# Optimization experiments

Hardware: AMD Instinct MI355X
Metric: run time of the kernel (lower is better)

The kernel has to match this reference:

```python
import jax, jax.numpy as jnp
import numpy as np

B = 2          # point clouds per batch
N_PER = 80000  # occupied voxels per cloud
D = 64         # voxel grid resolution
K = 27         # 3x3x3 kernel volume
EPS = 1e-5


def _build_maps():
    rng = np.random.RandomState(0)
    coords = []
    for b in range(B):
        flat = rng.choice(D ** 3, N_PER, replace=False)
        x = flat // (D * D); y = (flat // D) % D; z = flat % D
        coords.append(np.stack([np.full(N_PER, b, np.int64), x, y, z], 1))
    coords = np.concatenate(coords, 0)  # [N,4] (batch, x, y, z)

    def make_grid(c, Dd):
        g = np.full(B * Dd ** 3, -1, np.int64)
        key = ((c[:, 0] * Dd + c[:, 1]) * Dd + c[:, 2]) * Dd + c[:, 3]
        g[key] = np.arange(len(c))
        return g

    offsets = np.array([[dx, dy, dz] for dx in (-1, 0, 1) for dy in (-1, 0, 1) for dz in (-1, 0, 1)], np.int64)

    def kernel_map(c, g, Dd):
        # per kernel offset: (input_row, output_row) pairs, padded to M with sentinel n
        n = len(c)
        ins, outs = [], []
        for off in offsets:
            sc = c[:, 1:] + off
            valid = np.all((sc >= 0) & (sc < Dd), 1)
            key = ((c[:, 0] * Dd + sc[:, 0]) * Dd + sc[:, 1]) * Dd + sc[:, 2]
            row = np.where(valid, g[np.clip(key, 0, len(g) - 1)], -1)
            m = row >= 0
            ins.append(row[m]); outs.append(np.nonzero(m)[0])
        M = max(len(a) for a in ins)
        ki = np.full((K, M), n, np.int32); ko = np.full((K, M), n, np.int32)
        for k in range(K):
            ki[k, :len(ins[k])] = ins[k]; ko[k, :len(outs[k])] = outs[k]
        return ki, ko

    km_in, km_out = kernel_map(coords, make_grid(coords, D), D)

    # maxpool k2/s2: each voxel maps to exactly one pooled coordinate floor(c/2)
    Dp = D // 2
    pc = coords.copy(); pc[:, 1:] //= 2
    pkey = ((pc[:, 0] * Dp + pc[:, 1]) * Dp + pc[:, 2]) * Dp + pc[:, 3]
    ukey, pool_seg = np.unique(pkey, return_inverse=True)
    pz = ukey % Dp; py = (ukey // Dp) % Dp; px = (ukey // (Dp * Dp)) % Dp; pb = ukey // (Dp ** 3)
    pcoords = np.stack([pb, px, py, pz], 1)
    km2_in, km2_out = kernel_map(pcoords, make_grid(pcoords, Dp), Dp)
    return len(coords), len(pcoords), km_in, km_out, pool_seg.astype(np.int32), km2_in, km2_out


N, N_POOL, _KM_IN, _KM_OUT, _POOL_SEG, _KM2_IN, _KM2_OUT = _build_maps()


def setup_inputs() -> dict:
    key = jax.random.key(0)
    ks = jax.random.split(key, 4)
    f32 = jnp.float32
    return {
        "feats": jax.random.normal(ks[0], (N, 1), f32),
        "W1": jax.random.normal(ks[1], (K, 1, 64), f32) * 0.2,
        "b1": jnp.zeros((64,), f32),
        "g1": jnp.ones((64,), f32), "be1": jnp.zeros((64,), f32),
        "W2": jax.random.normal(ks[2], (K, 64, 64), f32) * 0.05,
        "b2": jnp.zeros((64,), f32),
        "g2": jnp.ones((64,), f32), "be2": jnp.zeros((64,), f32),
        "W3": jax.random.normal(ks[3], (K, 64, 128), f32) * 0.05,
        "b3": jnp.zeros((128,), f32),
        "g3": jnp.ones((128,), f32), "be3": jnp.zeros((128,), f32),
        "km_in": jnp.asarray(_KM_IN), "km_out": jnp.asarray(_KM_OUT),
        "pool_seg": jnp.asarray(_POOL_SEG),
        "km2_in": jnp.asarray(_KM2_IN), "km2_out": jnp.asarray(_KM2_OUT),
    }


def _sparse_conv(x, ki, ko, W, b):
    # gather-GEMM-scatter per kernel offset; sentinel index n hits padded zero row / dummy out row
    n = x.shape[0]
    xp = jnp.concatenate([x, jnp.zeros((1, x.shape[1]), x.dtype)], 0)
    out = jnp.zeros((n + 1, W.shape[2]), x.dtype)
    for k in range(K):
        out = out.at[ko[k]].add(xp[ki[k]] @ W[k])
    return out[:n] + b


def _bn_relu(x, g, b):
    # training-mode BatchNorm over all active voxels (biased variance), then ReLU
    mu = jnp.mean(x, 0)
    var = jnp.mean((x - mu) ** 2, 0)
    return jax.nn.relu(g * (x - mu) * jax.lax.rsqrt(var + EPS) + b)


def reference(feats, W1, b1, g1, be1, W2, b2, g2, be2, W3, b3, g3, be3,
              km_in, km_out, pool_seg, km2_in, km2_out):
    x = _bn_relu(_sparse_conv(feats, km_in, km_out, W1, b1), g1, be1)
    x = _bn_relu(_sparse_conv(x, km_in, km_out, W2, b2), g2, be2)
    # maxpool k2/s2: segment-max onto pooled coordinates
    x = jnp.full((N_POOL, x.shape[1]), -jnp.inf, x.dtype).at[pool_seg].max(x)
    x = _bn_relu(_sparse_conv(x, km2_in, km2_out, W3, b3), g3, be3)
    return x  # [N_POOL, 128]
```

## Files before the change

### kernel.cpp

```cpp
#include <hip/hip_runtime.h>

#define EPS 1e-5f
#define KK 27

typedef __bf16 bf16x8 __attribute__((ext_vector_type(8)));
typedef float f32x4 __attribute__((ext_vector_type(4)));

__device__ __forceinline__ unsigned short f2bf(float f) {
    union { float f; unsigned u; } v; v.f = f;
    unsigned r = v.u + 0x7fffu + ((v.u >> 16) & 1u);
    return (unsigned short)(r >> 16);
}
__device__ __forceinline__ float bf2f(unsigned short h) {
    union { unsigned u; float f; } v; v.u = ((unsigned)h) << 16; return v.f;
}

__device__ __forceinline__ f32x4 mfma16(bf16x8 a, bf16x8 b, f32x4 c) {
    return __builtin_amdgcn_mfma_f32_16x16x32_bf16(a, b, c, 0, 0, 0);
}

__global__ void fill_i32(int* __restrict__ p, long tot, int val) {
    long i = (long)blockIdx.x * blockDim.x + threadIdx.x;
    if (i < tot) p[i] = val;
}

__global__ void invert_map_g(const int* __restrict__ km_in, const int* __restrict__ km_out,
                             int* __restrict__ idxG, int M, int nrows) {
    long i = (long)blockIdx.x * blockDim.x + threadIdx.x;
    if (i >= (long)KK * M) return;
    int k = (int)(i / M);
    int ki = km_in[i];
    if (ki < nrows) {
        int ko = km_out[i];
        idxG[(long)(ko >> 5) * 1024 + k * 32 + (ko & 31)] = ki;
    }
}

__global__ void wt_frag(const float* __restrict__ W, unsigned short* __restrict__ Wt,
                        int Cin, int Cout) {
    long i = (long)blockIdx.x * blockDim.x + threadIdx.x;
    long tot = (long)KK * Cin * Cout;
    if (i >= tot) return;
    int k  = (int)(i / (Cin * Cout));
    int r  = (int)(i % (Cin * Cout));
    int ci = r / Cout, co = r % Cout;
    int t = co >> 4, m16 = co & 15;
    int s = ci >> 5, quad = (ci >> 3) & 3, j = ci & 7;
    int lane = quad * 16 + m16;
    long off = ((((long)k * (Cout >> 4) + t) * 2 + s) * 64 + lane) * 8 + j;
    Wt[off] = f2bf(W[i]);
}

__global__ void w1t_bf16(const float* __restrict__ W1, unsigned short* __restrict__ W1t) {
    int i = blockIdx.x * blockDim.x + threadIdx.x;
    if (i >= 64 * 32) return;
    int c = i / 32, kk = i % 32;
    W1t[i] = (kk < KK) ? f2bf(W1[kk * 64 + c]) : (unsigned short)0;
}

__global__ void stats_part(const float* __restrict__ p, int nblk, int width,
                           float* __restrict__ out) {
    int c = threadIdx.x;
    int b0 = blockIdx.x * 64;
    int b1 = b0 + 64 < nblk ? b0 + 64 : nblk;
    float acc = 0.f;
    for (int b = b0; b < b1; ++b) acc += p[(long)b * width + c];
    atomicAdd(&out[c], acc);
}

__global__ __launch_bounds__(256, 2) void conv1_mfma(const float* __restrict__ feats,
                                                     const unsigned short* __restrict__ W1t,
                                                     const int* __restrict__ idxG, int n,
                                                     unsigned short* __restrict__ out,
                                                     float* __restrict__ partial) {
    __shared__ __align__(16) int lidx[4][1024];
    __shared__ float sstat[4][128];
    int tid = threadIdx.x;
    int wave = tid >> 6, lane = tid & 63;
    int m16 = lane & 15, quad = lane >> 4;
    long tile = (long)blockIdx.x * 4 + wave;
    long j0 = tile * 32;
    bool valid = (j0 < n);
    long jb = valid ? (j0 >> 5) : 0;

    {
        float* z = (float*)sstat;
        #pragma unroll
        for (int i = 0; i < 2; ++i) z[tid + i * 256] = 0.f;
    }
    __syncthreads();

    {
        const int* src = idxG + jb * 1024;
        #pragma unroll
        for (int i = 0; i < 4; ++i)
            __builtin_amdgcn_global_load_lds(
                (const __attribute__((address_space(1))) unsigned*)(src + i * 256 + lane * 4),
                (__attribute__((address_space(3))) unsigned*)(&lidx[wave][i * 256]),
                16, 0, 0);
    }
    asm volatile("s_waitcnt vmcnt(0)" ::: "memory");
    const int* lip = &lidx[wave][0];

    int idx[2][8];
    #pragma unroll
    for (int i = 0; i < 8; ++i) {
        int kk = quad * 8 + i;
        bool kv = (kk < KK);
        idx[0][i] = (valid && kv) ? lip[kk * 32 + m16] : n;
        idx[1][i] = (valid && kv) ? lip[kk * 32 + 16 + m16] : n;
    }
    float f[2][8];
    #pragma unroll
    for (int i = 0; i < 8; ++i)
        #pragma unroll
        for (int t2 = 0; t2 < 2; ++t2) {
            int r = idx[t2][i];
            f[t2][i] = (r < n) ? feats[r] : 0.f;
        }

    union { bf16x8 v; unsigned short s[8]; } a[2];
    #pragma unroll
    for (int t2 = 0; t2 < 2; ++t2)
        #pragma unroll
        for (int i = 0; i < 8; ++i) a[t2].s[i] = f2bf(f[t2][i]);

    f32x4 acc[2][4];
    #pragma unroll
    for (int t2 = 0; t2 < 2; ++t2)
        #pragma unroll
        for (int t = 0; t < 4; ++t) acc[t2][t] = (f32x4){0.f, 0.f, 0.f, 0.f};

    const unsigned short* wb = W1t + quad * 8;
    #pragma unroll
    for (int t = 0; t < 4; ++t) {
        bf16x8 b = *(const bf16x8*)(wb + (t * 16 + m16) * 32);
        acc[0][t] = mfma16(a[0].v, b, acc[0][t]);
        acc[1][t] = mfma16(a[1].v, b, acc[1][t]);
    }

    asm volatile("" ::: "memory");
    unsigned short* sb = (unsigned short*)&lidx[wave][0];
    #pragma unroll
    for (int t2 = 0; t2 < 2; ++t2)
        #pragma unroll
        for (int t = 0; t < 4; ++t)
            #pragma unroll
            for (int r2 = 0; r2 < 4; ++r2)
                sb[(t2 * 16 + quad * 4 + r2) * 64 + t * 16 + m16] = f2bf(acc[t2][t][r2]);
    asm volatile("s_waitcnt lgkmcnt(0)" ::: "memory");
    #pragma unroll
    for (int i = 0; i < 4; ++i) {
        int row = i * 8 + (lane >> 3);
        long rr = j0 + row;
        if (rr < n)
            *(bf16x8*)(out + rr * 64 + (lane & 7) * 8) =
                *(const bf16x8*)(sb + row * 64 + (lane & 7) * 8);
    }

    #pragma unroll
    for (int t = 0; t < 4; ++t) {
        float s = 0.f, q = 0.f;
        #pragma unroll
        for (int t2 = 0; t2 < 2; ++t2)
            #pragma unroll
            for (int r2 = 0; r2 < 4; ++r2) { float v = acc[t2][t][r2]; s += v; q += v * v; }
        s += __shfl_xor(s, 16); q += __shfl_xor(q, 16);
        s += __shfl_xor(s, 32); q += __shfl_xor(q, 32);
        if (quad == 0) {
            sstat[wave][t * 16 + m16] = s;
            sstat[wave][64 + t * 16 + m16] = q;
        }
    }
    __syncthreads();
    if (tid < 128) {
        float p = sstat[0][tid] + sstat[1][tid] + sstat[2][tid] + sstat[3][tid];
        partial[(long)blockIdx.x * 128 + tid] = p;
    }
}

__global__ void bnrelu1_vec(unsigned short* __restrict__ x, const float* __restrict__ stats,
                            const float* __restrict__ g, const float* __restrict__ be, long n) {
    __shared__ float sc[64], sh[64];
    int tid = threadIdx.x;
    if (tid < 64) {
        float mu  = stats[tid] / (float)n;
        float var = stats[64 + tid] / (float)n - mu * mu;
        float s   = g[tid] * rsqrtf(var + EPS);
        sc[tid] = s; sh[tid] = be[tid] - mu * s;
    }
    __syncthreads();
    long i = (long)blockIdx.x * 256 + tid;
    long tot = (n + 1) * 8;
    if (i >= tot) return;
    long j = i >> 3; int c0 = (int)(i & 7) * 8;
    union { bf16x8 v; unsigned short s[8]; } u, o;
    if (j < n) {
        u.v = *(const bf16x8*)(x + j * 64 + c0);
        #pragma unroll
        for (int t = 0; t < 8; ++t) {
            float f = bf2f(u.s[t]) * sc[c0 + t] + sh[c0 + t];
            o.s[t] = f2bf(f > 0.f ? f : 0.f);
        }
    } else {
        #pragma unroll
        for (int t = 0; t < 8; ++t) o.s[t] = 0;
    }
    *(bf16x8*)(x + j * 64 + c0) = o.v;
}

template <int NCG, bool BF16OUT>
__global__ __launch_bounds__(256, 2) void conv64(const unsigned short* __restrict__ xin,
                                                 const unsigned short* __restrict__ Wt,
                                                 const int* __restrict__ idxG,
                                                 void* __restrict__ outv, int n,
                                                 float* __restrict__ partial) {
    constexpr int NT = 4;
    constexpr int COUTF = 64 * NCG;
    constexpr int SW = 2 * COUTF;
    constexpr long KSLICE = (long)COUTF * 128;
    __shared__ __align__(16) int lidx[4][2][1024];
    __shared__ float sstat[4][SW];

    int tid = threadIdx.x;
    int wave = tid >> 6, lane = tid & 63;
    int m16 = lane & 15, quad = lane >> 4;
    long gw = (long)blockIdx.x * 4 + wave;
    long tile = (NCG == 2) ? (gw >> 1) : gw;
    int cg = (NCG == 2) ? (int)(gw & 1) : 0;
    long j0 = tile * 64;
    bool v0 = (j0 < n), v1 = (j0 + 32 < n);
    long jb0 = v0 ? (j0 >> 5) : 0;
    long jb1 = v1 ? ((j0 >> 5) + 1) : 0;

    {
        float* z = (float*)sstat;
        #pragma unroll
        for (int i = 0; i < (4 * SW + 255) / 256; ++i) {
            int o = tid + i * 256;
            if (o < 4 * SW) z[o] = 0.f;
        }
    }
    __syncthreads();

    {
        const int* s0 = idxG + jb0 * 1024;
        const int* s1 = idxG + jb1 * 1024;
        #pragma unroll
        for (int i = 0; i < 4; ++i) {
            __builtin_amdgcn_global_load_lds(
                (const __attribute__((address_space(1))) unsigned*)(s0 + i * 256 + lane * 4),
                (__attribute__((address_space(3))) unsigned*)(&lidx[wave][0][i * 256]),
                16, 0, 0);
            __builtin_amdgcn_global_load_lds(
                (const __attribute__((address_space(1))) unsigned*)(s1 + i * 256 + lane * 4),
                (__attribute__((address_space(3))) unsigned*)(&lidx[wave][1][i * 256]),
                16, 0, 0);
        }
    }
    asm volatile("s_waitcnt vmcnt(0)" ::: "memory");
    const int* lip0 = &lidx[wave][0][m16];
    const int* lip1 = &lidx[wave][1][m16];

    const char* wlane = (const char*)Wt + (long)cg * (NT * 2048) + (long)lane * 16;
    const unsigned short* xq = xin + quad * 8;

    bf16x8 bB[2][8];
    bf16x8 aA[2][8];

    auto issueB = [&](int k, int ph) {
        const char* wk = wlane + (long)k * KSLICE;
        #pragma unroll
        for (int f = 0; f < 8; ++f)
            bB[ph][f] = *(const bf16x8*)(wk + f * 1024);
    };
    auto issueA = [&](int r00, int r01, int r10, int r11, int ph) {
        const unsigned short* a;
        a = xq + (long)r00 * 64; aA[ph][0] = *(const bf16x8*)a; aA[ph][1] = *(const bf16x8*)(a + 32);
        a = xq + (long)r01 * 64; aA[ph][2] = *(const bf16x8*)a; aA[ph][3] = *(const bf16x8*)(a + 32);
        a = xq + (long)r10 * 64; aA[ph][4] = *(const bf16x8*)a; aA[ph][5] = *(const bf16x8*)(a + 32);
        a = xq + (long)r11 * 64; aA[ph][6] = *(const bf16x8*)a; aA[ph][7] = *(const bf16x8*)(a + 32);
    };

    {
        int r00 = v0 ? lip0[0] : n, r01 = v0 ? lip0[16] : n;
        int r10 = v1 ? lip1[0] : n, r11 = v1 ? lip1[16] : n;
        issueB(0, 0); issueA(r00, r01, r10, r11, 0);
        r00 = v0 ? lip0[32] : n; r01 = v0 ? lip0[48] : n;
        r10 = v1 ? lip1[32] : n; r11 = v1 ? lip1[48] : n;
        issueB(1, 1); issueA(r00, r01, r10, r11, 1);
    }

    f32x4 acc[2][2][NT];
    #pragma unroll
    for (int u = 0; u < 2; ++u)
        #pragma unroll
        for (int h = 0; h < 2; ++h)
            #pragma unroll
            for (int t = 0; t < NT; ++t) acc[u][h][t] = (f32x4){0.f, 0.f, 0.f, 0.f};

    #pragma unroll
    for (int k = 0; k < KK; ++k) {
        int r00 = n, r01 = n, r10 = n, r11 = n;
        if (k + 2 < KK) {
            r00 = v0 ? lip0[(k + 2) * 32] : n;
            r01 = v0 ? lip0[(k + 2) * 32 + 16] : n;
            r10 = v1 ? lip1[(k + 2) * 32] : n;
            r11 = v1 ? lip1[(k + 2) * 32 + 16] : n;
        }
        if (k < KK - 1) asm volatile("s_waitcnt vmcnt(16)" ::: "memory");
        else            asm volatile("s_waitcnt vmcnt(0)" ::: "memory");
        __builtin_amdgcn_s_setprio(1);
        #pragma unroll
        for (int s = 0; s < 2; ++s)
            #pragma unroll
            for (int t = 0; t < NT; ++t) {
                bf16x8 b = bB[k & 1][t * 2 + s];
                acc[0][0][t] = mfma16(aA[k & 1][0 + s], b, acc[0][0][t]);
                acc[0][1][t] = mfma16(aA[k & 1][2 + s], b, acc[0][1][t]);
                acc[1][0][t] = mfma16(aA[k & 1][4 + s], b, acc[1][0][t]);
                acc[1][1][t] = mfma16(aA[k & 1][6 + s], b, acc[1][1][t]);
            }
        __builtin_amdgcn_s_setprio(0);
        if (k + 2 < KK) {
            issueB(k + 2, k & 1);
            issueA(r00, r01, r10, r11, k & 1);
        }
    }

    asm volatile("" ::: "memory");
    #pragma unroll
    for (int u = 0; u < 2; ++u) {
        if (BF16OUT) {
            unsigned short* sb = (unsigned short*)&lidx[wave][0][0];
            #pragma unroll
            for (int h = 0; h < 2; ++h)
                #pragma unroll
                for (int t = 0; t < NT; ++t)
                    #pragma unroll
                    for (int r2 = 0; r2 < 4; ++r2)
                        sb[(h * 16 + quad * 4 + r2) * 64 + t * 16 + m16] = f2bf(acc[u][h][t][r2]);
            asm volatile("s_waitcnt lgkmcnt(0)" ::: "memory");
            #pragma unroll
            for (int i = 0; i < 4; ++i) {
                int row = i * 8 + (lane >> 3);
                long rr = j0 + u * 32 + row;
                if (rr < n)
                    *(bf16x8*)((unsigned short*)outv + rr * 64 + (lane & 7) * 8) =
                        *(const bf16x8*)(sb + row * 64 + (lane & 7) * 8);
            }
            asm volatile("" ::: "memory");
        } else {
            float* sb = (float*)&lidx[wave][0][0];
            #pragma unroll
            for (int h = 0; h < 2; ++h)
                #pragma unroll
                for (int t = 0; t < NT; ++t)
                    #pragma unroll
                    for (int r2 = 0; r2 < 4; ++r2)
                        sb[(h * 16 + quad * 4 + r2) * 64 + t * 16 + m16] = acc[u][h][t][r2];
            asm volatile("s_waitcnt lgkmcnt(0)" ::: "memory");
            #pragma unroll
            for (int i = 0; i < 8; ++i) {
                int row = i * 4 + (lane >> 4);
                long rr = j0 + u * 32 + row;
                if (rr < n)
                    *(float4*)((float*)outv + rr * COUTF + cg * 64 + (lane & 15) * 4) =
                        *(const float4*)(sb + row * 64 + (lane & 15) * 4);
            }
            asm volatile("" ::: "memory");
        }
    }

    #pragma unroll
    for (int t = 0; t < NT; ++t) {
        float s = 0.f, q = 0.f;
        #pragma unroll
        for (int u = 0; u < 2; ++u)
            #pragma unroll
            for (int h = 0; h < 2; ++h)
                #pragma unroll
                for (int r2 = 0; r2 < 4; ++r2) { float v = acc[u][h][t][r2]; s += v; q += v * v; }
        s += __shfl_xor(s, 16); q += __shfl_xor(q, 16);
        s += __shfl_xor(s, 32); q += __shfl_xor(q, 32);
        if (quad == 0) {
            sstat[wave][cg * 64 + t * 16 + m16] = s;
            sstat[wave][COUTF + cg * 64 + t * 16 + m16] = q;
        }
    }
    __syncthreads();
    if (tid < SW) {
        float p = sstat[0][tid] + sstat[1][tid] + sstat[2][tid] + sstat[3][tid];
        partial[(long)blockIdx.x * SW + tid] = p;
    }
}

__global__ void pool_kernel(const unsigned short* __restrict__ x, const float* __restrict__ stats,
                            const float* __restrict__ g, const float* __restrict__ be,
                            const int* __restrict__ seg, long n, unsigned* __restrict__ pooled) {
    long j = (long)blockIdx.x * 4 + threadIdx.y;
    if (j >= n) return;
    int c = threadIdx.x;
    float mu  = stats[c] / (float)n;
    float var = stats[64 + c] / (float)n - mu * mu;
    float rs  = rsqrtf(var + EPS);
    float v   = g[c] * (bf2f(x[j * 64 + c]) - mu) * rs + be[c];
    if (v < 0.f) v = 0.f;
    atomicMax(&pooled[(long)seg[j] * 64 + c], __float_as_uint(v));
}

__global__ void pooled_bf16_vec(const unsigned* __restrict__ pooled, long np,
                                unsigned short* __restrict__ out) {
    long i = (long)blockIdx.x * 256 + threadIdx.x;
    long tot = (np + 1) * 8;
    if (i >= tot) return;
    long j = i >> 3; int c0 = (int)(i & 7) * 8;
    union { bf16x8 v; unsigned short s[8]; } o;
    if (j < np) {
        #pragma unroll
        for (int t = 0; t < 8; ++t)
            o.s[t] = f2bf(__uint_as_float(pooled[j * 64 + c0 + t]));
    } else {
        #pragma unroll
        for (int t = 0; t < 8; ++t) o.s[t] = 0;
    }
    *(bf16x8*)(out + j * 64 + c0) = o.v;
}

__global__ void bnrelu_out_vec(float* __restrict__ x, const float* __restrict__ stats,
                               const float* __restrict__ g, const float* __restrict__ be,
                               long n) {
    __shared__ float sc[128], sh[128];
    int tid = threadIdx.x;
    if (tid < 128) {
        float mu  = stats[tid] / (float)n;
        float var = stats[128 + tid] / (float)n - mu * mu;
        float s   = g[tid] * rsqrtf(var + EPS);
        sc[tid] = s; sh[tid] = be[tid] - mu * s;
    }
    __syncthreads();
    long i = (long)blockIdx.x * 256 + tid;
    long tot = n * 32;
    if (i >= tot) return;
    int c0 = (int)(i & 31) * 4;
    float4 v = ((float4*)x)[i];
    v.x = v.x * sc[c0]     + sh[c0];     v.x = v.x > 0.f ? v.x : 0.f;
    v.y = v.y * sc[c0 + 1] + sh[c0 + 1]; v.y = v.y > 0.f ? v.y : 0.f;
    v.z = v.z * sc[c0 + 2] + sh[c0 + 2]; v.z = v.z > 0.f ? v.z : 0.f;
    v.w = v.w * sc[c0 + 3] + sh[c0 + 3]; v.w = v.w > 0.f ? v.w : 0.f;
    ((float4*)x)[i] = v;
}

extern "C" void kernel_launch(void* const* d_in, const int* in_sizes, int n_in,
                              void* d_out, int out_size, void* d_ws, size_t ws_size,
                              hipStream_t stream) {
    const float* feats = (const float*)d_in[0];
    const float* W1  = (const float*)d_in[1];
    const float* g1  = (const float*)d_in[3];
    const float* be1 = (const float*)d_in[4];
    const float* W2  = (const float*)d_in[5];
    const float* g2  = (const float*)d_in[7];
    const float* be2 = (const float*)d_in[8];
    const float* W3  = (const float*)d_in[9];
    const float* g3  = (const float*)d_in[11];
    const float* be3 = (const float*)d_in[12];
    const int* km_in   = (const int*)d_in[13];
    const int* km_out  = (const int*)d_in[14];
    const int* pool_seg = (const int*)d_in[15];
    const int* km2_in  = (const int*)d_in[16];
    const int* km2_out = (const int*)d_in[17];

    const int n  = in_sizes[0];
    const int M  = in_sizes[13] / KK;
    const int np = out_size / 128;
    const int M2 = in_sizes[16] / KK;
    const long nb1 = n / 32 + 2;
    const long nb2 = np / 32 + 2;

    const int waves1 = (n + 31) / 32;
    const int nblk1  = (waves1 + 3) / 4;
    const int waves2 = (n + 63) / 64;
    const int nblk2  = (waves2 + 3) / 4;
    const int waves3 = ((np + 63) / 64) * 2;
    const int nblk3  = (waves3 + 3) / 4;


    char* ws = (char*)d_ws;
    size_t off = 0;
    auto alloc = [&](size_t bytes) -> char* {
        char* p = ws + off;
        off += (bytes + 255) & ~(size_t)255;
        return p;
    };
    int* idxG1 = (int*)alloc(nb1 * 4096);
    int* idxG2 = (int*)alloc(nb2 * 4096);
    unsigned short* W1t = (unsigned short*)alloc(64 * 32 * 2);
    unsigned short* W2t = (unsigned short*)alloc((size_t)KK * 64 * 64 * 2);
    unsigned short* W3t = (unsigned short*)alloc((size_t)KK * 128 * 64 * 2);
    float* stats = (float*)alloc(4096);
    unsigned short* x1n = (unsigned short*)alloc((size_t)(n + 1) * 64 * 2);
    unsigned short* x2r = (unsigned short*)alloc((size_t)n * 64 * 2);
    unsigned* pooled = (unsigned*)alloc((size_t)np * 64 * 4);
    unsigned short* xpn = (unsigned short*)alloc((size_t)(np + 1) * 64 * 2);
    float* part1 = (float*)alloc((size_t)nblk1 * 128 * 4);
    float* part2 = (float*)alloc((size_t)nblk2 * 128 * 4);
    float* part3 = (float*)alloc((size_t)nblk3 * 256 * 4);
    float* x3 = (float*)d_out;
    if (off > ws_size) return;

    float* stats1 = stats;
    float* stats2 = stats + 128;
    float* stats3 = stats + 256;

    hipMemsetAsync(stats, 0, 4096, stream);
    hipMemsetAsync(pooled, 0, (size_t)np * 64 * 4, stream);

    {
        long t1 = nb1 * 1024;
        fill_i32<<<(int)((t1 + 255) / 256), 256, 0, stream>>>(idxG1, t1, n);
        long t2 = nb2 * 1024;
        fill_i32<<<(int)((t2 + 255) / 256), 256, 0, stream>>>(idxG2, t2, np);
        long e1 = (long)KK * M;
        invert_map_g<<<(int)((e1 + 255) / 256), 256, 0, stream>>>(km_in, km_out, idxG1, M, n);
        long e2 = (long)KK * M2;
        invert_map_g<<<(int)((e2 + 255) / 256), 256, 0, stream>>>(km2_in, km2_out, idxG2, M2, np);
    }
    {
        w1t_bf16<<<8, 256, 0, stream>>>(W1, W1t);
        long t2 = (long)KK * 64 * 64;
        wt_frag<<<(int)((t2 + 255) / 256), 256, 0, stream>>>(W2, W2t, 64, 64);
        long t3 = (long)KK * 64 * 128;
        wt_frag<<<(int)((t3 + 255) / 256), 256, 0, stream>>>(W3, W3t, 64, 128);
    }

    conv1_mfma<<<nblk1, 256, 0, stream>>>(feats, W1t, idxG1, n, x1n, part1);
    stats_part<<<(nblk1 + 63) / 64, 128, 0, stream>>>(part1, nblk1, 128, stats1);
    {
        long tot = ((long)(n + 1) * 8 + 255) / 256;
        bnrelu1_vec<<<(int)tot, 256, 0, stream>>>(x1n, stats1, g1, be1, n);
    }
    conv64<1, true><<<nblk2, 256, 0, stream>>>(x1n, W2t, idxG1, x2r, n, part2);
    stats_part<<<(nblk2 + 63) / 64, 128, 0, stream>>>(part2, nblk2, 128, stats2);
    pool_kernel<<<(n + 3) / 4, dim3(64, 4), 0, stream>>>(x2r, stats2, g2, be2, pool_seg, n, pooled);
    {
        long tot = ((long)(np + 1) * 8 + 255) / 256;
        pooled_bf16_vec<<<(int)tot, 256, 0, stream>>>(pooled, np, xpn);
    }
    conv64<2, false><<<nblk3, 256, 0, stream>>>(xpn, W3t, idxG2, x3, np, part3);
    stats_part<<<(nblk3 + 63) / 64, 256, 0, stream>>>(part3, nblk3, 256, stats3);
    {
        long tot = ((long)np * 32 + 255) / 256;
        bnrelu_out_vec<<<(int)tot, 256, 0, stream>>>(x3, stats3, g3, be3, np);
    }
}
```

Measured before the change: 409.8 us.

## Reorder voxels by pool segment so max-pool is a contiguous segmented reduction

Builds a permutation that groups full-resolution voxels by their pooled cell (histogram, prefix scan, scatter), permutes the input features and remaps the first-level kernel map into that order. Conv1 and conv2 then run in permuted row order. Max-pool becomes a per-cell loop over contiguous rows that writes bf16 directly, replacing float atomicMax plus a separate conversion pass and memset. It also adds a block-index swizzle to the conv kernels. This costs several small extra launches for sorting, and scatter_perm fills rows within a segment in nondeterministic order.

```diff
diff --git a/kernel.cpp b/kernel.cpp
--- a/kernel.cpp
+++ b/kernel.cpp
@@ -19,9 +19,85 @@
     return __builtin_amdgcn_mfma_f32_16x16x32_bf16(a, b, c, 0, 0, 0);
 }
 
+__device__ __forceinline__ long swz_bid(long bid, long nwg) {
+    long q = nwg >> 3, r = nwg & 7;
+    long x = bid & 7, o = bid >> 3;
+    long base = (x < r) ? x * (q + 1) : r * (q + 1) + (x - r) * q;
+    return base + o;
+}
+
+__global__ void hist_seg(const int* __restrict__ seg, long n, int* __restrict__ cnt) {
+    long i = (long)blockIdx.x * 256 + threadIdx.x;
+    if (i < n) atomicAdd(&cnt[seg[i]], 1);
+}
+
+__global__ void scan_block256(const int* __restrict__ cnt, int np,
+                              int* __restrict__ excl, int* __restrict__ bsum) {
+    __shared__ int s[256];
+    int i = blockIdx.x * 256 + threadIdx.x;
+    int v = (i < np) ? cnt[i] : 0;
+    s[threadIdx.x] = v; __syncthreads();
+    #pragma unroll
+    for (int d = 1; d < 256; d <<= 1) {
+        int t = (threadIdx.x >= d) ? s[threadIdx.x - d] : 0;
+        __syncthreads();
+        s[threadIdx.x] += t;
+        __syncthreads();
+    }
+    if (i < np) excl[i] = s[threadIdx.x] - v;
+    if (threadIdx.x == 255) bsum[blockIdx.x] = s[255];
+}
+
+__global__ void scan_tops256(int* __restrict__ bsum, int nb) {
+    __shared__ int s[256];
+    int v = (threadIdx.x < nb) ? bsum[threadIdx.x] : 0;
+    s[threadIdx.x] = v; __syncthreads();
+    #pragma unroll
+    for (int d = 1; d < 256; d <<= 1) {
+        int t = (threadIdx.x >= d) ? s[threadIdx.x - d] : 0;
+        __syncthreads();
+        s[threadIdx.x] += t;
+        __syncthreads();
+    }
+    if (threadIdx.x < nb) bsum[threadIdx.x] = s[threadIdx.x] - v;
+}
+
+__global__ void scan_add(int* __restrict__ excl, const int* __restrict__ bsum, int np) {
+    int i = blockIdx.x * 256 + threadIdx.x;
+    if (i < np) excl[i] += bsum[blockIdx.x];
+}
+
+__global__ void scatter_perm(const int* __restrict__ seg, long n, int* __restrict__ ofs,
+                             int* __restrict__ perm, int* __restrict__ inv) {
+    long i = (long)blockIdx.x * 256 + threadIdx.x;
+    if (i >= n) return;
+    int p = atomicAdd(&ofs[seg[i]], 1);
+    perm[p] = (int)i;
+    inv[i] = p;
+}
+
+__global__ void permute_f32(const float* __restrict__ src, const int* __restrict__ perm,
+                            float* __restrict__ dst, long n) {
+    long i = (long)blockIdx.x * 256 + threadIdx.x;
+    if (i < n) dst[i] = src[perm[i]];
+}
+
 __global__ void fill_i32(int* __restrict__ p, long tot, int val) {
     long i = (long)blockIdx.x * blockDim.x + threadIdx.x;
     if (i < tot) p[i] = val;
+}
+
+__global__ void invert_map_p(const int* __restrict__ km_in, const int* __restrict__ km_out,
+                             const int* __restrict__ inv, int* __restrict__ idxG,
+                             int M, int nrows) {
+    long i = (long)blockIdx.x * blockDim.x + threadIdx.x;
+    if (i >= (long)KK * M) return;
+    int k = (int)(i / M);
+    int ki = km_in[i];
+    if (ki < nrows) {
+        int po = inv[km_out[i]];
+        idxG[(long)(po >> 5) * 1024 + k * 32 + (po & 31)] = inv[ki];
+    }
 }
 
 __global__ void invert_map_g(const int* __restrict__ km_in, const int* __restrict__ km_out,
@@ -78,7 +154,7 @@
     int tid = threadIdx.x;
     int wave = tid >> 6, lane = tid & 63;
     int m16 = lane & 15, quad = lane >> 4;
-    long tile = (long)blockIdx.x * 4 + wave;
+    long tile = swz_bid(blockIdx.x, gridDim.x) * 4 + wave;
     long j0 = tile * 32;
     bool valid = (j0 < n);
     long jb = valid ? (j0 >> 5) : 0;
@@ -225,7 +301,7 @@
     int tid = threadIdx.x;
     int wave = tid >> 6, lane = tid & 63;
     int m16 = lane & 15, quad = lane >> 4;
-    long gw = (long)blockIdx.x * 4 + wave;
+    long gw = swz_bid(blockIdx.x, gridDim.x) * 4 + wave;
     long tile = (NCG == 2) ? (gw >> 1) : gw;
     int cg = (NCG == 2) ? (int)(gw & 1) : 0;
     long j0 = tile * 64;
@@ -395,36 +471,27 @@
     }
 }
 
-__global__ void pool_kernel(const unsigned short* __restrict__ x, const float* __restrict__ stats,
+__global__ void pool_sorted(const unsigned short* __restrict__ x, const float* __restrict__ stats,
                             const float* __restrict__ g, const float* __restrict__ be,
-                            const int* __restrict__ seg, long n, unsigned* __restrict__ pooled) {
-    long j = (long)blockIdx.x * 4 + threadIdx.y;
-    if (j >= n) return;
-    int c = threadIdx.x;
+                            const int* __restrict__ ofs, const int* __restrict__ cnt,
+                            long n, int np, unsigned short* __restrict__ xpn) {
+    int wave = threadIdx.x >> 6, c = threadIdx.x & 63;
+    long p = (long)blockIdx.x * 4 + wave;
+    if (p > np) return;
+    if (p == np) { xpn[p * 64 + c] = 0; return; }
     float mu  = stats[c] / (float)n;
     float var = stats[64 + c] / (float)n - mu * mu;
-    float rs  = rsqrtf(var + EPS);
-    float v   = g[c] * (bf2f(x[j * 64 + c]) - mu) * rs + be[c];
-    if (v < 0.f) v = 0.f;
-    atomicMax(&pooled[(long)seg[j] * 64 + c], __float_as_uint(v));
-}
-
-__global__ void pooled_bf16_vec(const unsigned* __restrict__ pooled, long np,
-                                unsigned short* __restrict__ out) {
-    long i = (long)blockIdx.x * 256 + threadIdx.x;
-    long tot = (np + 1) * 8;
-    if (i >= tot) return;
-    long j = i >> 3; int c0 = (int)(i & 7) * 8;
-    union { bf16x8 v; unsigned short s[8]; } o;
-    if (j < np) {
-        #pragma unroll
-        for (int t = 0; t < 8; ++t)
-            o.s[t] = f2bf(__uint_as_float(pooled[j * 64 + c0 + t]));
-    } else {
-        #pragma unroll
-        for (int t = 0; t < 8; ++t) o.s[t] = 0;
-    }
-    *(bf16x8*)(out + j * 64 + c0) = o.v;
+    float sc  = g[c] * rsqrtf(var + EPS);
+    float sh  = be[c] - mu * sc;
+    int e = ofs[p];
+    int s = e - cnt[p];
+    float m = 0.f;
+    for (int r = s; r < e; ++r) {
+        float v = bf2f(x[(long)r * 64 + c]) * sc + sh;
+        if (v < 0.f) v = 0.f;
+        if (v > m) m = v;
+    }
+    xpn[p * 64 + c] = f2bf(m);
 }
 
 __global__ void bnrelu_out_vec(float* __restrict__ x, const float* __restrict__ stats,
@@ -500,11 +567,16 @@
     float* stats = (float*)alloc(4096);
     unsigned short* x1n = (unsigned short*)alloc((size_t)(n + 1) * 64 * 2);
     unsigned short* x2r = (unsigned short*)alloc((size_t)n * 64 * 2);
-    unsigned* pooled = (unsigned*)alloc((size_t)np * 64 * 4);
     unsigned short* xpn = (unsigned short*)alloc((size_t)(np + 1) * 64 * 2);
     float* part1 = (float*)alloc((size_t)nblk1 * 128 * 4);
     float* part2 = (float*)alloc((size_t)nblk2 * 128 * 4);
     float* part3 = (float*)alloc((size_t)nblk3 * 256 * 4);
+    int* cnt  = (int*)alloc((size_t)np * 4);
+    int* ofs  = (int*)alloc((size_t)np * 4);
+    int* bsum = (int*)alloc(256 * 4);
+    int* perm = (int*)alloc((size_t)n * 4);
+    int* invp = (int*)alloc((size_t)n * 4);
+    float* featp = (float*)alloc((size_t)n * 4);
     float* x3 = (float*)d_out;
     if (off > ws_size) return;
 
@@ -513,7 +585,18 @@
     float* stats3 = stats + 256;
 
     hipMemsetAsync(stats, 0, 4096, stream);
-    hipMemsetAsync(pooled, 0, (size_t)np * 64 * 4, stream);
+    hipMemsetAsync(cnt, 0, (size_t)np * 4, stream);
+
+    {
+        int nblk = (int)((n + 255) / 256);
+        hist_seg<<<nblk, 256, 0, stream>>>(pool_seg, n, cnt);
+        int nb = (np + 255) / 256;
+        scan_block256<<<nb, 256, 0, stream>>>(cnt, np, ofs, bsum);
+        scan_tops256<<<1, 256, 0, stream>>>(bsum, nb);
+        scan_add<<<nb, 256, 0, stream>>>(ofs, bsum, np);
+        scatter_perm<<<nblk, 256, 0, stream>>>(pool_seg, n, ofs, perm, invp);
+        permute_f32<<<nblk, 256, 0, stream>>>(feats, perm, featp, n);
+    }
 
     {
         long t1 = nb1 * 1024;
@@ -521,7 +604,7 @@
         long t2 = nb2 * 1024;
         fill_i32<<<(int)((t2 + 255) / 256), 256, 0, stream>>>(idxG2, t2, np);
         long e1 = (long)KK * M;
-        invert_map_g<<<(int)((e1 + 255) / 256), 256, 0, stream>>>(km_in, km_out, idxG1, M, n);
+        invert_map_p<<<(int)((e1 + 255) / 256), 256, 0, stream>>>(km_in, km_out, invp, idxG1, M, n);
         long e2 = (long)KK * M2;
         invert_map_g<<<(int)((e2 + 255) / 256), 256, 0, stream>>>(km2_in, km2_out, idxG2, M2, np);
     }
@@ -533,7 +616,7 @@
         wt_frag<<<(int)((t3 + 255) / 256), 256, 0, stream>>>(W3, W3t, 64, 128);
     }
 
-    conv1_mfma<<<nblk1, 256, 0, stream>>>(feats, W1t, idxG1, n, x1n, part1);
+    conv1_mfma<<<nblk1, 256, 0, stream>>>(featp, W1t, idxG1, n, x1n, part1);
     stats_part<<<(nblk1 + 63) / 64, 128, 0, stream>>>(part1, nblk1, 128, stats1);
     {
         long tot = ((long)(n + 1) * 8 + 255) / 256;
@@ -541,10 +624,9 @@
     }
     conv64<1, true><<<nblk2, 256, 0, stream>>>(x1n, W2t, idxG1, x2r, n, part2);
     stats_part<<<(nblk2 + 63) / 64, 128, 0, stream>>>(part2, nblk2, 128, stats2);
-    pool_kernel<<<(n + 3) / 4, dim3(64, 4), 0, stream>>>(x2r, stats2, g2, be2, pool_seg, n, pooled);
-    {
-        long tot = ((long)(np + 1) * 8 + 255) / 256;
-        pooled_bf16_vec<<<(int)tot, 256, 0, stream>>>(pooled, np, xpn);
+    {
+        int pblk = (np + 1 + 3) / 4;
+        pool_sorted<<<pblk, 256, 0, stream>>>(x2r, stats2, g2, be2, ofs, cnt, n, np, xpn);
     }
     conv64<2, false><<<nblk3, 256, 0, stream>>>(xpn, W3t, idxG2, x3, np, part3);
     stats_part<<<(nblk3 + 63) / 64, 256, 0, stream>>>(part3, nblk3, 256, stats3);
```

Measured after the change: 447.9 us. +9.3%, slower.

## Add triple-buffered LDS weight pipeline kernel for second sparse conv

Applied to the files above, without the earlier changes.

Adds a new conv_pipe kernel that streams each per-offset weight slice into LDS with a three-slot ring buffer via global_load_lds. It prefetches the gathered activation rows two kernel offsets ahead, so loads overlap the MFMA work. It replaces conv64<1> for the 64->64 layer, uses 32-row tiles per wave instead of 64, and drops an unneeded zeroing of sstat in conv1. The cost is more LDS per block (three weight slices) and a barrier per kernel offset, and smaller tiles mean each staged weight slice is reused less.

```diff
diff --git a/kernel.cpp b/kernel.cpp
--- a/kernel.cpp
+++ b/kernel.cpp
@@ -84,13 +84,6 @@
     long jb = valid ? (j0 >> 5) : 0;
 
     {
-        float* z = (float*)sstat;
-        #pragma unroll
-        for (int i = 0; i < 2; ++i) z[tid + i * 256] = 0.f;
-    }
-    __syncthreads();
-
-    {
         const int* src = idxG + jb * 1024;
         #pragma unroll
         for (int i = 0; i < 4; ++i)
@@ -207,6 +200,162 @@
         for (int t = 0; t < 8; ++t) o.s[t] = 0;
     }
     *(bf16x8*)(x + j * 64 + c0) = o.v;
+}
+
+template <int NT, bool BF16OUT>
+__global__ __launch_bounds__(256, 2) void conv_pipe(const unsigned short* __restrict__ xin,
+                                                    const unsigned short* __restrict__ Wt,
+                                                    const int* __restrict__ idxG,
+                                                    void* __restrict__ outv, int n,
+                                                    float* __restrict__ partial) {
+    constexpr int COUT = NT * 16;
+    constexpr int SLICE = COUT * 64 * 2;
+    constexpr int ROUNDS = SLICE / 4096;
+    __shared__ __align__(16) int lidx[4][1024];
+    __shared__ __align__(16) char bbuf[3][SLICE];
+    __shared__ float sstat[4][2 * COUT];
+
+    int tid = threadIdx.x;
+    int wave = tid >> 6, lane = tid & 63;
+    int m16 = lane & 15, quad = lane >> 4;
+    long tile = (long)blockIdx.x * 4 + wave;
+    long j0 = tile * 32;
+    bool valid = (j0 < n);
+    long jb = valid ? (j0 >> 5) : 0;
+
+    auto stageB = [&](int k, int slot) {
+        const char* src = (const char*)Wt + (long)k * SLICE;
+        #pragma unroll
+        for (int r = 0; r < ROUNDS; ++r)
+            __builtin_amdgcn_global_load_lds(
+                (const __attribute__((address_space(1))) unsigned*)(src + r * 4096 + wave * 1024 + lane * 16),
+                (__attribute__((address_space(3))) unsigned*)(&bbuf[slot][r * 4096 + wave * 1024]),
+                16, 0, 0);
+    };
+
+    {
+        const int* src = idxG + jb * 1024;
+        #pragma unroll
+        for (int i = 0; i < 4; ++i)
+            __builtin_amdgcn_global_load_lds(
+                (const __attribute__((address_space(1))) unsigned*)(src + i * 256 + lane * 4),
+                (__attribute__((address_space(3))) unsigned*)(&lidx[wave][i * 256]),
+                16, 0, 0);
+    }
+    stageB(0, 0);
+    if constexpr (ROUNDS == 2) asm volatile("s_waitcnt vmcnt(2)" ::: "memory");
+    else                       asm volatile("s_waitcnt vmcnt(4)" ::: "memory");
+
+    const int* lip = &lidx[wave][m16];
+    bf16x8 ar[3][2][2];
+    auto loadA = [&](int k, int slot) {
+        int r0 = valid ? lip[k * 32] : n;
+        int r1 = valid ? lip[k * 32 + 16] : n;
+        const unsigned short* a0 = xin + (long)r0 * 64 + quad * 8;
+        const unsigned short* a1 = xin + (long)r1 * 64 + quad * 8;
+        ar[slot][0][0] = *(const bf16x8*)a0;
+        ar[slot][0][1] = *(const bf16x8*)(a0 + 32);
+        ar[slot][1][0] = *(const bf16x8*)a1;
+        ar[slot][1][1] = *(const bf16x8*)(a1 + 32);
+    };
+    loadA(0, 0);
+    stageB(1, 1);
+    loadA(1, 1);
+
+    f32x4 acc[2][NT];
+    #pragma unroll
+    for (int t2 = 0; t2 < 2; ++t2)
+        #pragma unroll
+        for (int t = 0; t < NT; ++t) acc[t2][t] = (f32x4){0.f, 0.f, 0.f, 0.f};
+
+    #pragma unroll
+    for (int k = 0; k < KK; ++k) {
+        if (k < KK - 1) {
+            if constexpr (ROUNDS == 2) asm volatile("s_waitcnt vmcnt(6)" ::: "memory");
+            else                       asm volatile("s_waitcnt vmcnt(8)" ::: "memory");
+        } else {
+            asm volatile("s_waitcnt vmcnt(0)" ::: "memory");
+        }
+        __builtin_amdgcn_s_barrier();
+        __builtin_amdgcn_sched_barrier(0);
+        if (k + 2 < KK) {
+            stageB(k + 2, (k + 2) % 3);
+            loadA(k + 2, (k + 2) % 3);
+        }
+        const char* bs = &bbuf[k % 3][0];
+        __builtin_amdgcn_s_setprio(1);
+        #pragma unroll
+        for (int s = 0; s < 2; ++s)
+            #pragma unroll
+            for (int t = 0; t < NT; ++t) {
+                bf16x8 b = *(const bf16x8*)(bs + ((t * 2 + s) * 64 + lane) * 16);
+                acc[0][t] = mfma16(ar[k % 3][0][s], b, acc[0][t]);
+                acc[1][t] = mfma16(ar[k % 3][1][s], b, acc[1][t]);
+            }
+        __builtin_amdgcn_s_setprio(0);
+    }
+
+    asm volatile("" ::: "memory");
+    if (BF16OUT) {
+        unsigned short* sb = (unsigned short*)&lidx[wave][0];
+        #pragma unroll
+        for (int t2 = 0; t2 < 2; ++t2)
+            #pragma unroll
+            for (int t = 0; t < NT; ++t)
+                #pragma unroll
+                for (int r2 = 0; r2 < 4; ++r2)
+                    sb[(t2 * 16 + quad * 4 + r2) * 64 + t * 16 + m16] = f2bf(acc[t2][t][r2]);
+        asm volatile("s_waitcnt lgkmcnt(0)" ::: "memory");
+        #pragma unroll
+        for (int i = 0; i < 4; ++i) {
+            int row = i * 8 + (lane >> 3);
+            long rr = j0 + row;
+            if (rr < n)
+                *(bf16x8*)((unsigned short*)outv + rr * 64 + (lane & 7) * 8) =
+                    *(const bf16x8*)(sb + row * 64 + (lane & 7) * 8);
+        }
+        asm volatile("" ::: "memory");
+    } else {
+        float* sb = (float*)&lidx[wave][0];
+        #pragma unroll
+        for (int t2 = 0; t2 < 2; ++t2) {
+            #pragma unroll
+            for (int t = 0; t < NT; ++t)
+                #pragma unroll
+                for (int r2 = 0; r2 < 4; ++r2)
+                    sb[(quad * 4 + r2) * COUT + t * 16 + m16] = acc[t2][t][r2];
+            asm volatile("s_waitcnt lgkmcnt(0)" ::: "memory");
+            #pragma unroll
+            for (int i = 0; i < 4; ++i) {
+                int row = i * 4 + (lane >> 4);
+                long rr = j0 + t2 * 16 + row;
+                if (rr < n)
+                    *(float4*)((float*)outv + rr * COUT + (lane & 15) * 4) =
+                        *(const float4*)(sb + row * COUT + (lane & 15) * 4);
+            }
+            asm volatile("" ::: "memory");
+        }
+    }
+
+    #pragma unroll
+    for (int t = 0; t < NT; ++t) {
+        float s = 0.f, q = 0.f;
+        #pragma unroll
+        for (int t2 = 0; t2 < 2; ++t2)
+            #pragma unroll
+            for (int r2 = 0; r2 < 4; ++r2) { float v = acc[t2][t][r2]; s += v; q += v * v; }
+        s += __shfl_xor(s, 16); q += __shfl_xor(q, 16);
+        s += __shfl_xor(s, 32); q += __shfl_xor(q, 32);
+        if (quad == 0) {
+            sstat[wave][t * 16 + m16] = s;
+            sstat[wave][COUT + t * 16 + m16] = q;
+        }
+    }
+    __syncthreads();
+    if (tid < 2 * COUT) {
+        float p = sstat[0][tid] + sstat[1][tid] + sstat[2][tid] + sstat[3][tid];
+        partial[(long)blockIdx.x * (2 * COUT) + tid] = p;
+    }
 }
 
 template <int NCG, bool BF16OUT>
@@ -479,7 +628,7 @@
 
     const int waves1 = (n + 31) / 32;
     const int nblk1  = (waves1 + 3) / 4;
-    const int waves2 = (n + 63) / 64;
+    const int waves2 = (n + 31) / 32;
     const int nblk2  = (waves2 + 3) / 4;
     const int waves3 = ((np + 63) / 64) * 2;
     const int nblk3  = (waves3 + 3) / 4;
@@ -539,7 +688,7 @@
         long tot = ((long)(n + 1) * 8 + 255) / 256;
         bnrelu1_vec<<<(int)tot, 256, 0, stream>>>(x1n, stats1, g1, be1, n);
     }
-    conv64<1, true><<<nblk2, 256, 0, stream>>>(x1n, W2t, idxG1, x2r, n, part2);
+    conv_pipe<4, true><<<nblk2, 256, 0, stream>>>(x1n, W2t, idxG1, x2r, n, part2);
     stats_part<<<(nblk2 + 63) / 64, 128, 0, stream>>>(part2, nblk2, 128, stats2);
     pool_kernel<<<(n + 3) / 4, dim3(64, 4), 0, stream>>>(x2r, stats2, g2, be2, pool_seg, n, pooled);
     {
```

Measured after the change: 402.2 us. Within noise of the previous version (-1.9%).
